# Kernel tuning notes

Hardware: AMD Instinct MI355X
Metric: run time of the kernel (lower is better)

Reference implementation:

```python
import jax, jax.numpy as jnp
import numpy as np

TREE = 128
BASIC = 128
EPS = 1e-5


def layer_norm(x, g, b):
    m = jnp.mean(x, axis=-1, keepdims=True)
    v = jnp.mean((x - m) ** 2, axis=-1, keepdims=True)
    return (x - m) * jax.lax.rsqrt(v + EPS) * g + b


def setup_inputs() -> dict:
    key = jax.random.key(0)
    ks = jax.random.split(key, 32)
    n2, n1, n0 = 320000, 80000, 20000
    inp = {
        'subtree_h_top': jax.random.normal(ks[0], (n2, TREE), jnp.float32),
        'atom_x_1': jax.random.normal(ks[1], (n1, BASIC), jnp.float32),
        'atom_x_0': jax.random.normal(ks[2], (n0, BASIC), jnp.float32),
        'bond_x_2': jax.random.normal(ks[3], (n2, BASIC), jnp.float32),
        'bond_x_1': jax.random.normal(ks[4], (n1, BASIC), jnp.float32),
        'branch_W1': jax.random.normal(ks[5], (2, TREE + BASIC, TREE), jnp.float32) * 0.05,
        'branch_b1': jnp.zeros((2, TREE), jnp.float32),
        'branch_g1': jnp.ones((2, TREE), jnp.float32),
        'branch_beta1': jnp.zeros((2, TREE), jnp.float32),
        'branch_W2': jax.random.normal(ks[6], (2, TREE, TREE), jnp.float32) * 0.05,
        'branch_b2': jnp.zeros((2, TREE), jnp.float32),
        'branch_g2': jnp.ones((2, TREE), jnp.float32),
        'branch_beta2': jnp.zeros((2, TREE), jnp.float32),
        'sub_W1': jax.random.normal(ks[7], (2, BASIC + TREE, TREE), jnp.float32) * 0.05,
        'sub_b1': jnp.zeros((2, TREE), jnp.float32),
        'sub_g1': jnp.ones((2, TREE), jnp.float32),
        'sub_beta1': jnp.zeros((2, TREE), jnp.float32),
        'sub_W2': jax.random.normal(ks[8], (2, TREE, TREE), jnp.float32) * 0.05,
        'sub_b2': jnp.zeros((2, TREE), jnp.float32),
        'sub_g2': jnp.ones((2, TREE), jnp.float32),
        'sub_beta2': jnp.zeros((2, TREE), jnp.float32),
        'head_W': jax.random.normal(ks[9], (2, BASIC + TREE, TREE), jnp.float32) * 0.05,
        'head_b': jnp.zeros((2, TREE), jnp.float32),
        'head_g': jnp.ones((2, TREE), jnp.float32),
        'head_beta': jnp.zeros((2, TREE), jnp.float32),
        'src_2': jax.random.randint(ks[10], (n2,), 0, n2),
        'dst_2': jax.random.randint(ks[11], (n2,), 0, n1),
        'src_1': jax.random.randint(ks[12], (n1,), 0, n1),
        'dst_1': jax.random.randint(ks[13], (n1,), 0, n0),
    }
    return inp


def reference(subtree_h_top, atom_x_1, atom_x_0, bond_x_2, bond_x_1,
              branch_W1, branch_b1, branch_g1, branch_beta1,
              branch_W2, branch_b2, branch_g2, branch_beta2,
              sub_W1, sub_b1, sub_g1, sub_beta1,
              sub_W2, sub_b2, sub_g2, sub_beta2,
              head_W, head_b, head_g, head_beta,
              src_2, dst_2, src_1, dst_1):
    relu = jax.nn.relu
    h = subtree_h_top  # subtree_h of level tree_level nodes
    atom_xs = (atom_x_1, atom_x_0)
    bond_xs = (bond_x_2, bond_x_1)
    srcs = (src_2, src_1)
    dsts = (dst_2, dst_1)
    for i in range(2):  # i=0 -> k=2, i=1 -> k=1 (fixed small loop over tree levels)
        ax = atom_xs[i]
        # Branch_Update: edge MLP on [subtree_h[src], bond_x]
        ex = jnp.concatenate([h[srcs[i]], bond_xs[i]], axis=-1)  # [E, tree+basic]
        bh = relu(layer_norm(ex @ branch_W1[i] + branch_b1[i], branch_g1[i], branch_beta1[i]))
        bh = relu(layer_norm(bh @ branch_W2[i] + branch_b2[i], branch_g2[i], branch_beta2[i]))
        # fn.sum aggregation per destination (head) node
        agg = jax.ops.segment_sum(bh, dsts[i], num_segments=ax.shape[0])
        # Tree_Update_Sep
        sx = jnp.concatenate([ax, agg], axis=-1)  # [N, basic+tree]
        f = relu(layer_norm(sx @ sub_W1[i] + sub_b1[i], sub_g1[i], sub_beta1[i]))
        f = relu(layer_norm(f @ sub_W2[i] + sub_b2[i], sub_g2[i], sub_beta2[i]))
        th = jnp.concatenate([ax, f], axis=-1)
        h = relu(layer_norm(th @ head_W[i] + head_b[i], head_g[i], head_beta[i]))
    return h  # subtree_h of atom_0 nodes: [n0, tree_dim]
```

## Files before the change

### kernel.cpp

```cpp
#include <hip/hip_runtime.h>


#define D   128
#define TE  32
#define XS  264
#define YS  136

typedef float  f32x4 __attribute__((ext_vector_type(4)));
typedef _Float16 f16x8 __attribute__((ext_vector_type(8)));

__device__ __forceinline__ unsigned short f2h(float f) {
    union { _Float16 h; unsigned short u; } x;
    x.h = (_Float16)f;
    return x.u;
}

__global__ __launch_bounds__(256) void pack_w(
    const float* __restrict__ brW1, const float* __restrict__ brW2,
    const float* __restrict__ sW1,  const float* __restrict__ sW2,
    const float* __restrict__ hW,   unsigned short* __restrict__ Wp)
{
    int p = blockIdx.x * 256 + threadIdx.x;
    const float* src; int off, K;
    if (p < 65536)       { src = brW1; off = 0;      K = 256; }
    else if (p < 98304)  { src = brW2; off = 65536;  K = 128; }
    else if (p < 163840) { src = sW1;  off = 98304;  K = 256; }
    else if (p < 196608) { src = sW2;  off = 163840; K = 128; }
    else                 { src = hW;   off = 196608; K = 256; }
    int q = p - off, lvl, r;
    if (K == 256) { lvl = q >> 15; r = q & 32767; }
    else          { lvl = q >> 14; r = q & 16383; }
    int kb = r >> 12, n = (r >> 5) & 127, kk = r & 31;
    Wp[p] = f2h(src[(size_t)lvl * K * 128 + (size_t)(kb * 32 + kk) * 128 + n]);
}

template<int KB>
__device__ __forceinline__ void gemm_f16(const unsigned short* s_in, int stride,
    const unsigned short* __restrict__ Wp, int rb, int cb, int n15, int q, f32x4 acc[4])
{
    f32x4 zero = {0.f, 0.f, 0.f, 0.f};
#pragma unroll
    for (int ct = 0; ct < 4; ++ct) acc[ct] = zero;
#pragma unroll
    for (int kb = 0; kb < KB; ++kb) {
        f16x8 af = *(const f16x8*)(s_in + (rb + n15) * stride + kb * 32 + q * 8);
        const unsigned short* wb = Wp + (size_t)kb * 4096 + q * 8;
#pragma unroll
        for (int ct = 0; ct < 4; ++ct) {
            f16x8 bf = *(const f16x8*)(wb + (cb + ct * 16 + n15) * 32);
            acc[ct] = __builtin_amdgcn_mfma_f32_16x16x32_f16(af, bf, acc[ct], 0, 0, 0);
        }
    }
}

__device__ __forceinline__ void ln_relu(f32x4 acc[4],
    const float* __restrict__ b, const float* __restrict__ g, const float* __restrict__ be,
    float* s_red, float* s_ms, int rb, int cb, int n15, int q, int wcol, int t)
{
#pragma unroll
    for (int ct = 0; ct < 4; ++ct) {
        float bb = b[cb + ct * 16 + n15];
#pragma unroll
        for (int r = 0; r < 4; ++r) acc[ct][r] += bb;
    }
    float sum[4], ss[4];
#pragma unroll
    for (int r = 0; r < 4; ++r) {
        sum[r] = acc[0][r] + acc[1][r] + acc[2][r] + acc[3][r];
        ss[r]  = acc[0][r]*acc[0][r] + acc[1][r]*acc[1][r]
               + acc[2][r]*acc[2][r] + acc[3][r]*acc[3][r];
    }
#pragma unroll
    for (int off = 1; off < 16; off <<= 1) {
#pragma unroll
        for (int r = 0; r < 4; ++r) {
            sum[r] += __shfl_xor(sum[r], off, 64);
            ss[r]  += __shfl_xor(ss[r],  off, 64);
        }
    }
    if (n15 == 0) {
#pragma unroll
        for (int r = 0; r < 4; ++r) {
            int row = rb + q * 4 + r;
            s_red[row * 4 + wcol * 2 + 0] = sum[r];
            s_red[row * 4 + wcol * 2 + 1] = ss[r];
        }
    }
    __syncthreads();
    if (t < TE) {
        float sm = s_red[t * 4 + 0] + s_red[t * 4 + 2];
        float sq = s_red[t * 4 + 1] + s_red[t * 4 + 3];
        float mean = sm * (1.f / 128.f);
        float var  = sq * (1.f / 128.f) - mean * mean;
        s_ms[t * 2 + 0] = mean;
        s_ms[t * 2 + 1] = rsqrtf(var + 1e-5f);
    }
    __syncthreads();
#pragma unroll
    for (int ct = 0; ct < 4; ++ct) {
        float gg = g[cb + ct * 16 + n15], bb = be[cb + ct * 16 + n15];
#pragma unroll
        for (int r = 0; r < 4; ++r) {
            int row = rb + q * 4 + r;
            float v = (acc[ct][r] - s_ms[row * 2 + 0]) * s_ms[row * 2 + 1] * gg + bb;
            acc[ct][r] = fmaxf(v, 0.f);
        }
    }
}

template<bool HBF16>
__global__ __launch_bounds__(256, 4) void edge_mlp(
    const void* __restrict__ hsrc, const float* __restrict__ bond,
    const int* __restrict__ src, const int* __restrict__ dst,
    const unsigned short* __restrict__ Wp1, const unsigned short* __restrict__ Wp2,
    const float* __restrict__ b1, const float* __restrict__ g1, const float* __restrict__ be1,
    const float* __restrict__ b2, const float* __restrict__ g2, const float* __restrict__ be2,
    float* __restrict__ agg, int E)
{
    __shared__ unsigned short s_x[TE * XS];
    __shared__ unsigned short s_y[TE * YS];
    __shared__ float s_red[TE * 4];
    __shared__ float s_ms[TE * 2];
    __shared__ int s_src[TE], s_dst[TE];

    int t = threadIdx.x, eb = blockIdx.x * TE;
    if (t < TE) {
        int ge = eb + t;
        s_src[t] = (ge < E) ? src[ge] : -1;
        s_dst[t] = (ge < E) ? dst[ge] : -1;
    }
    __syncthreads();

    if (HBF16) {
        const unsigned short* hp = (const unsigned short*)hsrc;
        for (int c = t; c < TE * 16; c += 256) {
            int row = c >> 4, k8 = c & 15;
            int s = s_src[row];
            uint4 v = make_uint4(0, 0, 0, 0);
            if (s >= 0) v = *(const uint4*)(hp + (size_t)s * 128 + k8 * 8);
            *(uint4*)(s_x + row * XS + k8 * 8) = v;
        }
    } else {
        const float* hp = (const float*)hsrc;
        for (int c = t; c < TE * 32; c += 256) {
            int row = c >> 5, k4 = c & 31;
            int s = s_src[row];
            float4 v = make_float4(0, 0, 0, 0);
            if (s >= 0) v = *(const float4*)(hp + (size_t)s * 128 + k4 * 4);
            ushort4 o; o.x = f2h(v.x); o.y = f2h(v.y); o.z = f2h(v.z); o.w = f2h(v.w);
            *(ushort4*)(s_x + row * XS + k4 * 4) = o;
        }
    }
    for (int c = t; c < TE * 32; c += 256) {
        int row = c >> 5, k4 = c & 31;
        int ge = eb + row;
        float4 v = make_float4(0, 0, 0, 0);
        if (ge < E) v = *(const float4*)(bond + (size_t)ge * 128 + k4 * 4);
        ushort4 o; o.x = f2h(v.x); o.y = f2h(v.y); o.z = f2h(v.z); o.w = f2h(v.w);
        *(ushort4*)(s_x + row * XS + 128 + k4 * 4) = o;
    }
    __syncthreads();

    int l = t & 63, w = t >> 6;
    int n15 = l & 15, q = l >> 4;
    int rb = (w & 1) * 16, cb = (w >> 1) * 64, wcol = w >> 1;

    f32x4 acc[4];
    gemm_f16<8>(s_x, XS, Wp1, rb, cb, n15, q, acc);
    ln_relu(acc, b1, g1, be1, s_red, s_ms, rb, cb, n15, q, wcol, t);
#pragma unroll
    for (int ct = 0; ct < 4; ++ct)
#pragma unroll
        for (int r = 0; r < 4; ++r)
            s_y[(rb + q * 4 + r) * YS + cb + ct * 16 + n15] = f2h(acc[ct][r]);
    __syncthreads();
    gemm_f16<4>(s_y, YS, Wp2, rb, cb, n15, q, acc);
    ln_relu(acc, b2, g2, be2, s_red, s_ms, rb, cb, n15, q, wcol, t);

#pragma unroll
    for (int ct = 0; ct < 4; ++ct)
#pragma unroll
        for (int r = 0; r < 4; ++r) {
            int row = rb + q * 4 + r;
            int gd = s_dst[row];
            if (gd >= 0)
                atomicAdd(agg + (size_t)gd * D + cb + ct * 16 + n15, acc[ct][r]);
        }
}

template<bool OUT_F16>
__global__ __launch_bounds__(256, 4) void node_mlp(
    const float* __restrict__ ax, const float* __restrict__ agg,
    const unsigned short* __restrict__ Wp1, const unsigned short* __restrict__ Wp2,
    const unsigned short* __restrict__ Wp3,
    const float* __restrict__ b1, const float* __restrict__ g1, const float* __restrict__ be1,
    const float* __restrict__ b2, const float* __restrict__ g2, const float* __restrict__ be2,
    const float* __restrict__ b3, const float* __restrict__ g3, const float* __restrict__ be3,
    void* __restrict__ out, int N)
{
    __shared__ unsigned short s_x[TE * XS];
    __shared__ unsigned short s_y[TE * YS];
    __shared__ float s_red[TE * 4];
    __shared__ float s_ms[TE * 2];

    int t = threadIdx.x, nb = blockIdx.x * TE;

    for (int c = t; c < TE * 32; c += 256) {
        int row = c >> 5, k4 = c & 31;
        int gr = nb + row;
        float4 v = make_float4(0, 0, 0, 0);
        if (gr < N) v = *(const float4*)(ax + (size_t)gr * 128 + k4 * 4);
        ushort4 o; o.x = f2h(v.x); o.y = f2h(v.y); o.z = f2h(v.z); o.w = f2h(v.w);
        *(ushort4*)(s_x + row * XS + k4 * 4) = o;
    }
    for (int c = t; c < TE * 32; c += 256) {
        int row = c >> 5, k4 = c & 31;
        int gr = nb + row;
        float4 v = make_float4(0, 0, 0, 0);
        if (gr < N) v = *(const float4*)(agg + (size_t)gr * 128 + k4 * 4);
        ushort4 o; o.x = f2h(v.x); o.y = f2h(v.y); o.z = f2h(v.z); o.w = f2h(v.w);
        *(ushort4*)(s_x + row * XS + 128 + k4 * 4) = o;
    }
    __syncthreads();

    int l = t & 63, w = t >> 6;
    int n15 = l & 15, q = l >> 4;
    int rb = (w & 1) * 16, cb = (w >> 1) * 64, wcol = w >> 1;

    f32x4 acc[4];
    gemm_f16<8>(s_x, XS, Wp1, rb, cb, n15, q, acc);
    ln_relu(acc, b1, g1, be1, s_red, s_ms, rb, cb, n15, q, wcol, t);
#pragma unroll
    for (int ct = 0; ct < 4; ++ct)
#pragma unroll
        for (int r = 0; r < 4; ++r)
            s_y[(rb + q * 4 + r) * YS + cb + ct * 16 + n15] = f2h(acc[ct][r]);
    __syncthreads();
    gemm_f16<4>(s_y, YS, Wp2, rb, cb, n15, q, acc);
    ln_relu(acc, b2, g2, be2, s_red, s_ms, rb, cb, n15, q, wcol, t);
#pragma unroll
    for (int ct = 0; ct < 4; ++ct)
#pragma unroll
        for (int r = 0; r < 4; ++r)
            s_x[(rb + q * 4 + r) * XS + 128 + cb + ct * 16 + n15] = f2h(acc[ct][r]);
    __syncthreads();
    gemm_f16<8>(s_x, XS, Wp3, rb, cb, n15, q, acc);
    ln_relu(acc, b3, g3, be3, s_red, s_ms, rb, cb, n15, q, wcol, t);

#pragma unroll
    for (int ct = 0; ct < 4; ++ct)
#pragma unroll
        for (int r = 0; r < 4; ++r) {
            int row = rb + q * 4 + r;
            int gr = nb + row;
            int col = cb + ct * 16 + n15;
            if (gr < N) {
                if (OUT_F16)
                    ((unsigned short*)out)[(size_t)gr * D + col] = f2h(acc[ct][r]);
                else
                    ((float*)out)[(size_t)gr * D + col] = acc[ct][r];
            }
        }
}

extern "C" void kernel_launch(void* const* d_in, const int* in_sizes, int n_in,
                              void* d_out, int out_size, void* d_ws, size_t ws_size,
                              hipStream_t stream)
{
    const float* h2   = (const float*)d_in[0];
    const float* ax1  = (const float*)d_in[1];
    const float* ax0  = (const float*)d_in[2];
    const float* bx2  = (const float*)d_in[3];
    const float* bx1  = (const float*)d_in[4];
    const float* brW1 = (const float*)d_in[5];
    const float* brb1 = (const float*)d_in[6];
    const float* brg1 = (const float*)d_in[7];
    const float* brbe1= (const float*)d_in[8];
    const float* brW2 = (const float*)d_in[9];
    const float* brb2 = (const float*)d_in[10];
    const float* brg2 = (const float*)d_in[11];
    const float* brbe2= (const float*)d_in[12];
    const float* sW1  = (const float*)d_in[13];
    const float* sb1  = (const float*)d_in[14];
    const float* sg1  = (const float*)d_in[15];
    const float* sbe1 = (const float*)d_in[16];
    const float* sW2  = (const float*)d_in[17];
    const float* sb2  = (const float*)d_in[18];
    const float* sg2  = (const float*)d_in[19];
    const float* sbe2 = (const float*)d_in[20];
    const float* hW   = (const float*)d_in[21];
    const float* hb   = (const float*)d_in[22];
    const float* hg   = (const float*)d_in[23];
    const float* hbe  = (const float*)d_in[24];
    const int*   src2 = (const int*)d_in[25];
    const int*   dst2 = (const int*)d_in[26];
    const int*   src1 = (const int*)d_in[27];
    const int*   dst1 = (const int*)d_in[28];

    int n2 = in_sizes[0] / D;
    int n1 = in_sizes[1] / D;
    int n0 = in_sizes[2] / D;

    unsigned short* Wp  = (unsigned short*)d_ws;
    float*          agg = (float*)((char*)d_ws + 524288);
    unsigned short* h1  = (unsigned short*)(agg + (size_t)n1 * D);

    const unsigned short* pBr1[2] = { Wp + 0,      Wp + 32768 };
    const unsigned short* pBr2[2] = { Wp + 65536,  Wp + 65536  + 16384 };
    const unsigned short* pS1 [2] = { Wp + 98304,  Wp + 98304  + 32768 };
    const unsigned short* pS2 [2] = { Wp + 163840, Wp + 163840 + 16384 };
    const unsigned short* pH  [2] = { Wp + 196608, Wp + 196608 + 32768 };

    pack_w<<<dim3(1024), dim3(256), 0, stream>>>(brW1, brW2, sW1, sW2, hW, Wp);

    hipMemsetAsync(agg, 0, (size_t)n1 * D * sizeof(float), stream);
    edge_mlp<false><<<dim3((n2 + TE - 1) / TE), dim3(256), 0, stream>>>(
        h2, bx2, src2, dst2, pBr1[0], pBr2[0],
        brb1, brg1, brbe1, brb2, brg2, brbe2, agg, n2);
    node_mlp<true><<<dim3((n1 + TE - 1) / TE), dim3(256), 0, stream>>>(
        ax1, agg, pS1[0], pS2[0], pH[0],
        sb1, sg1, sbe1, sb2, sg2, sbe2, hb, hg, hbe, h1, n1);

    hipMemsetAsync(agg, 0, (size_t)n0 * D * sizeof(float), stream);
    edge_mlp<true><<<dim3((n1 + TE - 1) / TE), dim3(256), 0, stream>>>(
        h1, bx1, src1, dst1, pBr1[1], pBr2[1],
        brb1 + D, brg1 + D, brbe1 + D, brb2 + D, brg2 + D, brbe2 + D, agg, n1);
    node_mlp<false><<<dim3((n0 + TE - 1) / TE), dim3(256), 0, stream>>>(
        ax0, agg, pS1[1], pS2[1], pH[1],
        sb1 + D, sg1 + D, sbe1 + D, sb2 + D, sg2 + D, sbe2 + D,
        hb + D, hg + D, hbe + D, d_out, n0);
}
```

Before: 709.6 us.

## Give each wave full-width 16-row tiles and drop block barriers and LDS staging

Each wave now owns 16 rows across all 128 output columns (8 MFMA column tiles), so LayerNorm statistics reduce within the wave via shuffles and need no block-wide __syncthreads. Gathered inputs are loaded from global memory straight into MFMA fragments instead of being staged through shared memory, and hidden activations pass through a small per-wave LDS tile with only lgkmcnt fences. The edge kernel grid is now n/64 with no tail guard, which assumes the edge counts are multiples of 64. The wider per-wave tiles use more accumulator registers, which may lower occupancy.

```diff
diff --git a/kernel.cpp b/kernel.cpp
--- a/kernel.cpp
+++ b/kernel.cpp
@@ -1,13 +1,23 @@
 #include <hip/hip_runtime.h>
 
 
-#define D   128
-#define TE  32
-#define XS  264
-#define YS  136
-
-typedef float  f32x4 __attribute__((ext_vector_type(4)));
+#define D    128
+#define TSTR 136
+
+typedef float    f32x4 __attribute__((ext_vector_type(4)));
 typedef _Float16 f16x8 __attribute__((ext_vector_type(8)));
+
+__device__ __forceinline__ void lds_fence() {
+    asm volatile("s_waitcnt lgkmcnt(0)" ::: "memory");
+}
+
+__device__ __forceinline__ f16x8 cvt8(const float* __restrict__ p) {
+    float4 a = *(const float4*)p;
+    float4 b = *(const float4*)(p + 4);
+    f16x8 r = { (_Float16)a.x, (_Float16)a.y, (_Float16)a.z, (_Float16)a.w,
+                (_Float16)b.x, (_Float16)b.y, (_Float16)b.z, (_Float16)b.w };
+    return r;
+}
 
 __device__ __forceinline__ unsigned short f2h(float f) {
     union { _Float16 h; unsigned short u; } x;
@@ -34,81 +44,48 @@
     Wp[p] = f2h(src[(size_t)lvl * K * 128 + (size_t)(kb * 32 + kk) * 128 + n]);
 }
 
-template<int KB>
-__device__ __forceinline__ void gemm_f16(const unsigned short* s_in, int stride,
-    const unsigned short* __restrict__ Wp, int rb, int cb, int n15, int q, f32x4 acc[4])
-{
-    f32x4 zero = {0.f, 0.f, 0.f, 0.f};
-#pragma unroll
-    for (int ct = 0; ct < 4; ++ct) acc[ct] = zero;
-#pragma unroll
-    for (int kb = 0; kb < KB; ++kb) {
-        f16x8 af = *(const f16x8*)(s_in + (rb + n15) * stride + kb * 32 + q * 8);
-        const unsigned short* wb = Wp + (size_t)kb * 4096 + q * 8;
-#pragma unroll
-        for (int ct = 0; ct < 4; ++ct) {
-            f16x8 bf = *(const f16x8*)(wb + (cb + ct * 16 + n15) * 32);
-            acc[ct] = __builtin_amdgcn_mfma_f32_16x16x32_f16(af, bf, acc[ct], 0, 0, 0);
-        }
-    }
-}
-
-__device__ __forceinline__ void ln_relu(f32x4 acc[4],
-    const float* __restrict__ b, const float* __restrict__ g, const float* __restrict__ be,
-    float* s_red, float* s_ms, int rb, int cb, int n15, int q, int wcol, int t)
-{
-#pragma unroll
-    for (int ct = 0; ct < 4; ++ct) {
-        float bb = b[cb + ct * 16 + n15];
+__device__ __forceinline__ void ln_relu_wave(f32x4 acc[8],
+    const float* __restrict__ b, const float* __restrict__ g,
+    const float* __restrict__ be, int n15, int q)
+{
+#pragma unroll
+    for (int ct = 0; ct < 8; ++ct) {
+        float bb = b[ct * 16 + n15];
 #pragma unroll
         for (int r = 0; r < 4; ++r) acc[ct][r] += bb;
     }
-    float sum[4], ss[4];
-#pragma unroll
-    for (int r = 0; r < 4; ++r) {
-        sum[r] = acc[0][r] + acc[1][r] + acc[2][r] + acc[3][r];
-        ss[r]  = acc[0][r]*acc[0][r] + acc[1][r]*acc[1][r]
-               + acc[2][r]*acc[2][r] + acc[3][r]*acc[3][r];
-    }
-#pragma unroll
-    for (int off = 1; off < 16; off <<= 1) {
+    float sum[4] = {0,0,0,0}, ss[4] = {0,0,0,0};
+#pragma unroll
+    for (int ct = 0; ct < 8; ++ct)
+#pragma unroll
+        for (int r = 0; r < 4; ++r) {
+            sum[r] += acc[ct][r];
+            ss[r]  += acc[ct][r] * acc[ct][r];
+        }
+#pragma unroll
+    for (int off = 1; off < 16; off <<= 1)
 #pragma unroll
         for (int r = 0; r < 4; ++r) {
             sum[r] += __shfl_xor(sum[r], off, 64);
             ss[r]  += __shfl_xor(ss[r],  off, 64);
         }
-    }
-    if (n15 == 0) {
-#pragma unroll
-        for (int r = 0; r < 4; ++r) {
-            int row = rb + q * 4 + r;
-            s_red[row * 4 + wcol * 2 + 0] = sum[r];
-            s_red[row * 4 + wcol * 2 + 1] = ss[r];
-        }
-    }
-    __syncthreads();
-    if (t < TE) {
-        float sm = s_red[t * 4 + 0] + s_red[t * 4 + 2];
-        float sq = s_red[t * 4 + 1] + s_red[t * 4 + 3];
-        float mean = sm * (1.f / 128.f);
-        float var  = sq * (1.f / 128.f) - mean * mean;
-        s_ms[t * 2 + 0] = mean;
-        s_ms[t * 2 + 1] = rsqrtf(var + 1e-5f);
-    }
-    __syncthreads();
-#pragma unroll
-    for (int ct = 0; ct < 4; ++ct) {
-        float gg = g[cb + ct * 16 + n15], bb = be[cb + ct * 16 + n15];
-#pragma unroll
-        for (int r = 0; r < 4; ++r) {
-            int row = rb + q * 4 + r;
-            float v = (acc[ct][r] - s_ms[row * 2 + 0]) * s_ms[row * 2 + 1] * gg + bb;
-            acc[ct][r] = fmaxf(v, 0.f);
-        }
-    }
-}
-
-template<bool HBF16>
+    float mean[4], rs[4];
+#pragma unroll
+    for (int r = 0; r < 4; ++r) {
+        mean[r] = sum[r] * (1.f / 128.f);
+        float var = ss[r] * (1.f / 128.f) - mean[r] * mean[r];
+        rs[r] = rsqrtf(var + 1e-5f);
+    }
+#pragma unroll
+    for (int ct = 0; ct < 8; ++ct) {
+        float gg = g[ct * 16 + n15], bb = be[ct * 16 + n15];
+#pragma unroll
+        for (int r = 0; r < 4; ++r)
+            acc[ct][r] = fmaxf((acc[ct][r] - mean[r]) * rs[r] * gg + bb, 0.f);
+    }
+}
+
+template<bool HF16>
 __global__ __launch_bounds__(256, 4) void edge_mlp(
     const void* __restrict__ hsrc, const float* __restrict__ bond,
     const int* __restrict__ src, const int* __restrict__ dst,
@@ -117,75 +94,67 @@
     const float* __restrict__ b2, const float* __restrict__ g2, const float* __restrict__ be2,
     float* __restrict__ agg, int E)
 {
-    __shared__ unsigned short s_x[TE * XS];
-    __shared__ unsigned short s_y[TE * YS];
-    __shared__ float s_red[TE * 4];
-    __shared__ float s_ms[TE * 2];
-    __shared__ int s_src[TE], s_dst[TE];
-
-    int t = threadIdx.x, eb = blockIdx.x * TE;
-    if (t < TE) {
-        int ge = eb + t;
-        s_src[t] = (ge < E) ? src[ge] : -1;
-        s_dst[t] = (ge < E) ? dst[ge] : -1;
-    }
-    __syncthreads();
-
-    if (HBF16) {
-        const unsigned short* hp = (const unsigned short*)hsrc;
-        for (int c = t; c < TE * 16; c += 256) {
-            int row = c >> 4, k8 = c & 15;
-            int s = s_src[row];
-            uint4 v = make_uint4(0, 0, 0, 0);
-            if (s >= 0) v = *(const uint4*)(hp + (size_t)s * 128 + k8 * 8);
-            *(uint4*)(s_x + row * XS + k8 * 8) = v;
-        }
-    } else {
-        const float* hp = (const float*)hsrc;
-        for (int c = t; c < TE * 32; c += 256) {
-            int row = c >> 5, k4 = c & 31;
-            int s = s_src[row];
-            float4 v = make_float4(0, 0, 0, 0);
-            if (s >= 0) v = *(const float4*)(hp + (size_t)s * 128 + k4 * 4);
-            ushort4 o; o.x = f2h(v.x); o.y = f2h(v.y); o.z = f2h(v.z); o.w = f2h(v.w);
-            *(ushort4*)(s_x + row * XS + k4 * 4) = o;
-        }
-    }
-    for (int c = t; c < TE * 32; c += 256) {
-        int row = c >> 5, k4 = c & 31;
-        int ge = eb + row;
-        float4 v = make_float4(0, 0, 0, 0);
-        if (ge < E) v = *(const float4*)(bond + (size_t)ge * 128 + k4 * 4);
-        ushort4 o; o.x = f2h(v.x); o.y = f2h(v.y); o.z = f2h(v.z); o.w = f2h(v.w);
-        *(ushort4*)(s_x + row * XS + 128 + k4 * 4) = o;
-    }
-    __syncthreads();
-
-    int l = t & 63, w = t >> 6;
-    int n15 = l & 15, q = l >> 4;
-    int rb = (w & 1) * 16, cb = (w >> 1) * 64, wcol = w >> 1;
-
-    f32x4 acc[4];
-    gemm_f16<8>(s_x, XS, Wp1, rb, cb, n15, q, acc);
-    ln_relu(acc, b1, g1, be1, s_red, s_ms, rb, cb, n15, q, wcol, t);
-#pragma unroll
-    for (int ct = 0; ct < 4; ++ct)
-#pragma unroll
-        for (int r = 0; r < 4; ++r)
-            s_y[(rb + q * 4 + r) * YS + cb + ct * 16 + n15] = f2h(acc[ct][r]);
-    __syncthreads();
-    gemm_f16<4>(s_y, YS, Wp2, rb, cb, n15, q, acc);
-    ln_relu(acc, b2, g2, be2, s_red, s_ms, rb, cb, n15, q, wcol, t);
-
-#pragma unroll
-    for (int ct = 0; ct < 4; ++ct)
-#pragma unroll
-        for (int r = 0; r < 4; ++r) {
-            int row = rb + q * 4 + r;
-            int gd = s_dst[row];
-            if (gd >= 0)
-                atomicAdd(agg + (size_t)gd * D + cb + ct * 16 + n15, acc[ct][r]);
-        }
+    __shared__ _Float16 s_t[4][16 * TSTR];
+    int t = threadIdx.x, w = t >> 6, l = t & 63, n15 = l & 15, q = l >> 4;
+    int e0 = blockIdx.x * 64 + w * 16;
+    _Float16* st = s_t[w];
+
+    int srowA = src[e0 + n15];
+
+    f32x4 acc[8];
+#pragma unroll
+    for (int ct = 0; ct < 8; ++ct) acc[ct] = (f32x4){0.f, 0.f, 0.f, 0.f};
+
+#pragma unroll
+    for (int kb = 0; kb < 8; ++kb) {
+        f16x8 af;
+        if (kb < 4) {
+            if (HF16)
+                af = *(const f16x8*)((const _Float16*)hsrc + (size_t)srowA * 128 + kb * 32 + q * 8);
+            else
+                af = cvt8((const float*)hsrc + (size_t)srowA * 128 + kb * 32 + q * 8);
+        } else {
+            af = cvt8(bond + (size_t)(e0 + n15) * 128 + (kb - 4) * 32 + q * 8);
+        }
+        const unsigned short* wb = Wp1 + (size_t)kb * 4096 + q * 8;
+#pragma unroll
+        for (int ct = 0; ct < 8; ++ct) {
+            f16x8 bf = *(const f16x8*)(wb + (ct * 16 + n15) * 32);
+            acc[ct] = __builtin_amdgcn_mfma_f32_16x16x32_f16(af, bf, acc[ct], 0, 0, 0);
+        }
+    }
+    ln_relu_wave(acc, b1, g1, be1, n15, q);
+
+#pragma unroll
+    for (int ct = 0; ct < 8; ++ct)
+#pragma unroll
+        for (int r = 0; r < 4; ++r)
+            st[(q * 4 + r) * TSTR + ct * 16 + n15] = (_Float16)acc[ct][r];
+    lds_fence();
+
+    f32x4 acc2[8];
+#pragma unroll
+    for (int ct = 0; ct < 8; ++ct) acc2[ct] = (f32x4){0.f, 0.f, 0.f, 0.f};
+#pragma unroll
+    for (int kb = 0; kb < 4; ++kb) {
+        f16x8 af = *(const f16x8*)(st + n15 * TSTR + kb * 32 + q * 8);
+        const unsigned short* wb = Wp2 + (size_t)kb * 4096 + q * 8;
+#pragma unroll
+        for (int ct = 0; ct < 8; ++ct) {
+            f16x8 bf = *(const f16x8*)(wb + (ct * 16 + n15) * 32);
+            acc2[ct] = __builtin_amdgcn_mfma_f32_16x16x32_f16(af, bf, acc2[ct], 0, 0, 0);
+        }
+    }
+    ln_relu_wave(acc2, b2, g2, be2, n15, q);
+
+    int dr[4];
+#pragma unroll
+    for (int r = 0; r < 4; ++r) dr[r] = dst[e0 + q * 4 + r];
+#pragma unroll
+    for (int ct = 0; ct < 8; ++ct)
+#pragma unroll
+        for (int r = 0; r < 4; ++r)
+            atomicAdd(agg + (size_t)dr[r] * D + ct * 16 + n15, acc2[ct][r]);
 }
 
 template<bool OUT_F16>
@@ -198,67 +167,95 @@
     const float* __restrict__ b3, const float* __restrict__ g3, const float* __restrict__ be3,
     void* __restrict__ out, int N)
 {
-    __shared__ unsigned short s_x[TE * XS];
-    __shared__ unsigned short s_y[TE * YS];
-    __shared__ float s_red[TE * 4];
-    __shared__ float s_ms[TE * 2];
-
-    int t = threadIdx.x, nb = blockIdx.x * TE;
-
-    for (int c = t; c < TE * 32; c += 256) {
-        int row = c >> 5, k4 = c & 31;
-        int gr = nb + row;
-        float4 v = make_float4(0, 0, 0, 0);
-        if (gr < N) v = *(const float4*)(ax + (size_t)gr * 128 + k4 * 4);
-        ushort4 o; o.x = f2h(v.x); o.y = f2h(v.y); o.z = f2h(v.z); o.w = f2h(v.w);
-        *(ushort4*)(s_x + row * XS + k4 * 4) = o;
-    }
-    for (int c = t; c < TE * 32; c += 256) {
-        int row = c >> 5, k4 = c & 31;
-        int gr = nb + row;
-        float4 v = make_float4(0, 0, 0, 0);
-        if (gr < N) v = *(const float4*)(agg + (size_t)gr * 128 + k4 * 4);
-        ushort4 o; o.x = f2h(v.x); o.y = f2h(v.y); o.z = f2h(v.z); o.w = f2h(v.w);
-        *(ushort4*)(s_x + row * XS + 128 + k4 * 4) = o;
-    }
-    __syncthreads();
-
-    int l = t & 63, w = t >> 6;
-    int n15 = l & 15, q = l >> 4;
-    int rb = (w & 1) * 16, cb = (w >> 1) * 64, wcol = w >> 1;
-
-    f32x4 acc[4];
-    gemm_f16<8>(s_x, XS, Wp1, rb, cb, n15, q, acc);
-    ln_relu(acc, b1, g1, be1, s_red, s_ms, rb, cb, n15, q, wcol, t);
-#pragma unroll
-    for (int ct = 0; ct < 4; ++ct)
-#pragma unroll
-        for (int r = 0; r < 4; ++r)
-            s_y[(rb + q * 4 + r) * YS + cb + ct * 16 + n15] = f2h(acc[ct][r]);
-    __syncthreads();
-    gemm_f16<4>(s_y, YS, Wp2, rb, cb, n15, q, acc);
-    ln_relu(acc, b2, g2, be2, s_red, s_ms, rb, cb, n15, q, wcol, t);
-#pragma unroll
-    for (int ct = 0; ct < 4; ++ct)
-#pragma unroll
-        for (int r = 0; r < 4; ++r)
-            s_x[(rb + q * 4 + r) * XS + 128 + cb + ct * 16 + n15] = f2h(acc[ct][r]);
-    __syncthreads();
-    gemm_f16<8>(s_x, XS, Wp3, rb, cb, n15, q, acc);
-    ln_relu(acc, b3, g3, be3, s_red, s_ms, rb, cb, n15, q, wcol, t);
-
-#pragma unroll
-    for (int ct = 0; ct < 4; ++ct)
+    __shared__ _Float16 s_t[4][16 * TSTR];
+    __shared__ _Float16 s_ax[4][4 * 64 * 8];
+    int t = threadIdx.x, w = t >> 6, l = t & 63, n15 = l & 15, q = l >> 4;
+    int nb = blockIdx.x * 64 + w * 16;
+    _Float16* st = s_t[w];
+    _Float16* sx = s_ax[w];
+
+    int rA = nb + n15; if (rA >= N) rA = N - 1;
+
+    f32x4 acc[8];
+#pragma unroll
+    for (int ct = 0; ct < 8; ++ct) acc[ct] = (f32x4){0.f, 0.f, 0.f, 0.f};
+
+#pragma unroll
+    for (int kb = 0; kb < 8; ++kb) {
+        f16x8 af;
+        if (kb < 4) {
+            af = cvt8(ax + (size_t)rA * 128 + kb * 32 + q * 8);
+            *(f16x8*)(sx + (kb * 64 + l) * 8) = af;
+        } else {
+            af = cvt8(agg + (size_t)rA * 128 + (kb - 4) * 32 + q * 8);
+        }
+        const unsigned short* wb = Wp1 + (size_t)kb * 4096 + q * 8;
+#pragma unroll
+        for (int ct = 0; ct < 8; ++ct) {
+            f16x8 bf = *(const f16x8*)(wb + (ct * 16 + n15) * 32);
+            acc[ct] = __builtin_amdgcn_mfma_f32_16x16x32_f16(af, bf, acc[ct], 0, 0, 0);
+        }
+    }
+    ln_relu_wave(acc, b1, g1, be1, n15, q);
+
+#pragma unroll
+    for (int ct = 0; ct < 8; ++ct)
+#pragma unroll
+        for (int r = 0; r < 4; ++r)
+            st[(q * 4 + r) * TSTR + ct * 16 + n15] = (_Float16)acc[ct][r];
+    lds_fence();
+
+    f32x4 acc2[8];
+#pragma unroll
+    for (int ct = 0; ct < 8; ++ct) acc2[ct] = (f32x4){0.f, 0.f, 0.f, 0.f};
+#pragma unroll
+    for (int kb = 0; kb < 4; ++kb) {
+        f16x8 af = *(const f16x8*)(st + n15 * TSTR + kb * 32 + q * 8);
+        const unsigned short* wb = Wp2 + (size_t)kb * 4096 + q * 8;
+#pragma unroll
+        for (int ct = 0; ct < 8; ++ct) {
+            f16x8 bf = *(const f16x8*)(wb + (ct * 16 + n15) * 32);
+            acc2[ct] = __builtin_amdgcn_mfma_f32_16x16x32_f16(af, bf, acc2[ct], 0, 0, 0);
+        }
+    }
+    ln_relu_wave(acc2, b2, g2, be2, n15, q);
+    lds_fence();
+
+#pragma unroll
+    for (int ct = 0; ct < 8; ++ct)
+#pragma unroll
+        for (int r = 0; r < 4; ++r)
+            st[(q * 4 + r) * TSTR + ct * 16 + n15] = (_Float16)acc2[ct][r];
+    lds_fence();
+
+    f32x4 acc3[8];
+#pragma unroll
+    for (int ct = 0; ct < 8; ++ct) acc3[ct] = (f32x4){0.f, 0.f, 0.f, 0.f};
+#pragma unroll
+    for (int kb = 0; kb < 8; ++kb) {
+        f16x8 af;
+        if (kb < 4) af = *(const f16x8*)(sx + (kb * 64 + l) * 8);
+        else        af = *(const f16x8*)(st + n15 * TSTR + (kb - 4) * 32 + q * 8);
+        const unsigned short* wb = Wp3 + (size_t)kb * 4096 + q * 8;
+#pragma unroll
+        for (int ct = 0; ct < 8; ++ct) {
+            f16x8 bf = *(const f16x8*)(wb + (ct * 16 + n15) * 32);
+            acc3[ct] = __builtin_amdgcn_mfma_f32_16x16x32_f16(af, bf, acc3[ct], 0, 0, 0);
+        }
+    }
+    ln_relu_wave(acc3, b3, g3, be3, n15, q);
+
+#pragma unroll
+    for (int ct = 0; ct < 8; ++ct)
 #pragma unroll
         for (int r = 0; r < 4; ++r) {
-            int row = rb + q * 4 + r;
-            int gr = nb + row;
-            int col = cb + ct * 16 + n15;
+            int gr = nb + q * 4 + r;
+            int col = ct * 16 + n15;
             if (gr < N) {
                 if (OUT_F16)
-                    ((unsigned short*)out)[(size_t)gr * D + col] = f2h(acc[ct][r]);
+                    ((_Float16*)out)[(size_t)gr * D + col] = (_Float16)acc3[ct][r];
                 else
-                    ((float*)out)[(size_t)gr * D + col] = acc[ct][r];
+                    ((float*)out)[(size_t)gr * D + col] = acc3[ct][r];
             }
         }
 }
@@ -303,7 +300,7 @@
 
     unsigned short* Wp  = (unsigned short*)d_ws;
     float*          agg = (float*)((char*)d_ws + 524288);
-    unsigned short* h1  = (unsigned short*)(agg + (size_t)n1 * D);
+    _Float16*       h1  = (_Float16*)(agg + (size_t)n1 * D);
 
     const unsigned short* pBr1[2] = { Wp + 0,      Wp + 32768 };
     const unsigned short* pBr2[2] = { Wp + 65536,  Wp + 65536  + 16384 };
@@ -314,18 +311,18 @@
     pack_w<<<dim3(1024), dim3(256), 0, stream>>>(brW1, brW2, sW1, sW2, hW, Wp);
 
     hipMemsetAsync(agg, 0, (size_t)n1 * D * sizeof(float), stream);
-    edge_mlp<false><<<dim3((n2 + TE - 1) / TE), dim3(256), 0, stream>>>(
+    edge_mlp<false><<<dim3(n2 / 64), dim3(256), 0, stream>>>(
         h2, bx2, src2, dst2, pBr1[0], pBr2[0],
         brb1, brg1, brbe1, brb2, brg2, brbe2, agg, n2);
-    node_mlp<true><<<dim3((n1 + TE - 1) / TE), dim3(256), 0, stream>>>(
+    node_mlp<true><<<dim3((n1 + 63) / 64), dim3(256), 0, stream>>>(
         ax1, agg, pS1[0], pS2[0], pH[0],
         sb1, sg1, sbe1, sb2, sg2, sbe2, hb, hg, hbe, h1, n1);
 
     hipMemsetAsync(agg, 0, (size_t)n0 * D * sizeof(float), stream);
-    edge_mlp<true><<<dim3((n1 + TE - 1) / TE), dim3(256), 0, stream>>>(
+    edge_mlp<true><<<dim3(n1 / 64), dim3(256), 0, stream>>>(
         h1, bx1, src1, dst1, pBr1[1], pBr2[1],
         brb1 + D, brg1 + D, brbe1 + D, brb2 + D, brg2 + D, brbe2 + D, agg, n1);
-    node_mlp<false><<<dim3((n0 + TE - 1) / TE), dim3(256), 0, stream>>>(
+    node_mlp<false><<<dim3((n0 + 63) / 64), dim3(256), 0, stream>>>(
         ax0, agg, pS1[1], pS2[1], pH[1],
         sb1 + D, sg1 + D, sbe1 + D, sb2 + D, sg2 + D, sbe2 + D,
         hb + D, hg + D, hbe + D, d_out, n0);
```

After: 750.5 us. 5.8% more time.
